# Kernel tuning notes

Hardware: AMD Instinct MI355X
Metric: run time of the kernel (lower is better)

The kernel has to match this reference:

```python
import jax, jax.numpy as jnp
import numpy as np

B, H, SQ, SKV, D = 2, 16, 2048, 2048, 64
SCALE = 8  # sqrt(head_dim)


def setup_inputs() -> dict:
    key = jax.random.key(0)
    kq, kk, kv, km = jax.random.split(key, 4)
    q = jax.random.normal(kq, (B, H, SQ, D), dtype=jnp.float32)
    k = jax.random.normal(kk, (B, H, SKV, D), dtype=jnp.float32)
    v = jax.random.normal(kv, (B, H, SKV, D), dtype=jnp.float32)
    mask = jax.random.normal(km, (1, 1, SQ, SKV), dtype=jnp.float32)
    return {"q": q, "k": k, "v": v, "mask": mask, "scale": SCALE}


def reference(q, k, v, mask, scale):
    # scores: [B, H, SQ, SKV]
    scores = jnp.einsum("bhqd,bhkd->bhqk", q, k) / scale
    scores = scores + mask  # broadcast additive mask
    probs = jax.nn.softmax(scores, axis=-1)
    # hidden: [B, H, SQ, D]
    return jnp.einsum("bhqk,bhkd->bhqd", probs, v)
```

## Files before the change

kernel.cpp:

```cpp
#include <hip/hip_runtime.h>
#include <hip/hip_bf16.h>

#define NB 2
#define NH 16
#define NSQ 2048
#define NSKV 2048
#define ND 64
#define NT (NSKV / 64)
#define LOG2E 1.4426950408889634f
#define BHSTRIDE (NSKV * ND)

typedef __attribute__((ext_vector_type(8))) short bf16x8;
typedef __attribute__((ext_vector_type(4))) float f32x4;
typedef __attribute__((address_space(1))) const unsigned gas_u32;
typedef __attribute__((address_space(3))) unsigned las_u32;

__device__ __forceinline__ short f2bf(float x) {
  union { float f; unsigned u; } c; c.f = x;
  unsigned r = c.u + 0x7fffu + ((c.u >> 16) & 1u);
  return (short)(r >> 16);
}
__device__ __forceinline__ unsigned pack_bf2(float lo, float hi) {
  union { __hip_bfloat162 h; unsigned u; } c;
  c.h = __float22bfloat162_rn(float2{lo, hi});
  return c.u;
}
__device__ __forceinline__ float u2f(unsigned u) {
  union { unsigned u; float f; } c; c.u = u; return c.f;
}
__device__ __forceinline__ float exp2_fast(float x) {
#if __has_builtin(__builtin_amdgcn_exp2f)
  return __builtin_amdgcn_exp2f(x);
#else
  return exp2f(x);
#endif
}

__device__ __forceinline__ int kvmap(int x) {
  return (x & 3) | (((x >> 4) & 1) << 2) | (((x >> 2) & 1) << 3)
       | (((x >> 3) & 1) << 4) | (x & 32);
}

__global__ void prep_all(const float* __restrict__ K, const float* __restrict__ V,
                         const float* __restrict__ M, short* __restrict__ Kp,
                         short* __restrict__ Vp, unsigned short* __restrict__ Mt) {
  __shared__ float T[64][65];
  const int tile = blockIdx.x;
  const int bh   = blockIdx.y;
  const int kv0  = tile * 64;
  const int t    = (int)threadIdx.x;

  {
    const float* src = V + ((size_t)bh * NSKV + kv0) * ND;
#pragma unroll
    for (int i = 0; i < 4; ++i) {
      float4 v = *(const float4*)(src + (size_t)((t >> 4) + 16 * i) * ND + (t & 15) * 4);
      T[(t >> 4) + 16 * i][(t & 15) * 4 + 0] = v.x;
      T[(t >> 4) + 16 * i][(t & 15) * 4 + 1] = v.y;
      T[(t >> 4) + 16 * i][(t & 15) * 4 + 2] = v.z;
      T[(t >> 4) + 16 * i][(t & 15) * 4 + 3] = v.w;
    }
    __syncthreads();
    const int d = t >> 2, c = t & 3;
    bf16x8 w0, w1;
#pragma unroll
    for (int j = 0; j < 8; ++j) w0[j] = f2bf(T[c * 16 + j][d]);
#pragma unroll
    for (int j = 0; j < 8; ++j) w1[j] = f2bf(T[c * 16 + 8 + j][d]);
    const int frag  = (d >> 4) * 2 + (c >> 1);
    const int lane0 = (((2 * c) & 3) << 4) | (d & 15);
    const int lane1 = (((2 * c + 1) & 3) << 4) | (d & 15);
    short* dstb = Vp + (size_t)bh * BHSTRIDE + (size_t)tile * 4096 + frag * 512;
    *(bf16x8*)(dstb + lane0 * 8) = w0;
    *(bf16x8*)(dstb + lane1 * 8) = w1;
  }

#pragma unroll
  for (int h = 0; h < 2; ++h) {
    const int u    = t + h * 256;
    const int nt   = u >> 7, kc = (u >> 6) & 1, lane = u & 63;
    const int prow = nt * 16 + (lane & 15);
    const float* src = K + ((size_t)bh * NSKV + kv0 + kvmap(prow)) * ND
                         + kc * 32 + (lane >> 4) * 8;
    float4 a = *(const float4*)src, b = *(const float4*)(src + 4);
    bf16x8 w;
    w[0]=f2bf(a.x); w[1]=f2bf(a.y); w[2]=f2bf(a.z); w[3]=f2bf(a.w);
    w[4]=f2bf(b.x); w[5]=f2bf(b.y); w[6]=f2bf(b.z); w[7]=f2bf(b.w);
    *(bf16x8*)(Kp + (size_t)bh * BHSTRIDE + (size_t)tile * 4096 + u * 8) = w;
  }

  {
    const int rl = t >> 4, c = t & 15;
    const int nt   = 2 * (c >> 3) + (c & 1);
    const int lq   = (c >> 1) & 3;
    const int lane = lq * 16 + rl;
#pragma unroll
    for (int i = 0; i < 4; ++i) {
      const int qt  = bh * 4 + i;
      const int row = qt * 16 + rl;
      float4 v = *(const float4*)(M + (size_t)row * NSKV + tile * 64 + c * 4);
      ushort4 o;
      o.x = (unsigned short)f2bf(LOG2E * v.x);
      o.y = (unsigned short)f2bf(LOG2E * v.y);
      o.z = (unsigned short)f2bf(LOG2E * v.z);
      o.w = (unsigned short)f2bf(LOG2E * v.w);
      *(ushort4*)(Mt + (((size_t)qt * 32 + tile) * 64 + lane) * 16 + nt * 4) = o;
    }
  }
}

__global__ __launch_bounds__(256, 2)
void attn_fwd(const float* __restrict__ Q, const short* __restrict__ Kp,
              const short* __restrict__ Vp, const unsigned short* __restrict__ Mt,
              const void* __restrict__ scale_p, float* __restrict__ O)
{
  const int lin = (int)blockIdx.x + ((int)blockIdx.y << 4);
  const int swz = ((lin & 7) << 6) | (lin >> 3);
  const int qb  = swz & 15;
  const int bh  = swz >> 4;

  const int tid = (int)threadIdx.x;
  const int wv  = tid >> 6;
  const int ln  = tid & 63;
  const int l16 = ln & 15;
  const int lq  = ln >> 4;

  float scale_v;
  {
    union { int i; float f; } u;
    u.i = ((const int*)scale_p)[0];
    float af = fabsf(u.f);
    scale_v = (af >= 1e-6f && af <= 1e6f) ? u.f : (float)u.i;
  }
  const float qmul = LOG2E / scale_v;

  const int q0 = qb * 128;
  const short* Kb = Kp + (size_t)bh * BHSTRIDE;
  const short* Vb = Vp + (size_t)bh * BHSTRIDE;

  __shared__ short Kl[2][4096];
  __shared__ short Vl[2][4096];

  bf16x8 qf[2][2];
#pragma unroll
  for (int qs = 0; qs < 2; ++qs) {
    const float* qrow = Q + ((size_t)bh * NSQ + q0 + wv * 32 + qs * 16 + l16) * ND;
#pragma unroll
    for (int kc = 0; kc < 2; ++kc) {
      const float4* p = (const float4*)(qrow + kc * 32 + lq * 8);
      float4 a = p[0], b = p[1];
      bf16x8 f;
      f[0]=f2bf(a.x*qmul); f[1]=f2bf(a.y*qmul); f[2]=f2bf(a.z*qmul); f[3]=f2bf(a.w*qmul);
      f[4]=f2bf(b.x*qmul); f[5]=f2bf(b.y*qmul); f[6]=f2bf(b.z*qmul); f[7]=f2bf(b.w*qmul);
      qf[qs][kc] = f;
    }
  }

  f32x4 oa[2][4];
  f32x4 lacc[2];
#pragma unroll
  for (int qs = 0; qs < 2; ++qs) {
#pragma unroll
    for (int dt = 0; dt < 4; ++dt) { f32x4 z = {0.f,0.f,0.f,0.f}; oa[qs][dt] = z; }
    f32x4 z = {0.f,0.f,0.f,0.f}; lacc[qs] = z;
  }

  bf16x8 ones;
#pragma unroll
  for (int j = 0; j < 8; ++j) ones[j] = (short)0x3F80;

  const unsigned short* M0 = Mt + (size_t)(qb * 8 + wv * 2) * 32768 + (size_t)ln * 16;
  const unsigned short* M1 = M0 + 32768;

  auto mload = [&](int t, float4* mf0, float4* mf1) {
    const unsigned short* p0 = M0 + (size_t)t * 1024;
    const unsigned short* p1 = M1 + (size_t)t * 1024;
    uint4 a0 = *(const uint4*)p0, b0 = *(const uint4*)(p0 + 8);
    uint4 a1 = *(const uint4*)p1, b1 = *(const uint4*)(p1 + 8);
    const unsigned u0[8] = {a0.x,a0.y,a0.z,a0.w,b0.x,b0.y,b0.z,b0.w};
    const unsigned u1[8] = {a1.x,a1.y,a1.z,a1.w,b1.x,b1.y,b1.z,b1.w};
#pragma unroll
    for (int nt = 0; nt < 4; ++nt) {
      mf0[nt] = float4{u2f(u0[nt*2] << 16), u2f(u0[nt*2] & 0xffff0000u),
                       u2f(u0[nt*2+1] << 16), u2f(u0[nt*2+1] & 0xffff0000u)};
      mf1[nt] = float4{u2f(u1[nt*2] << 16), u2f(u1[nt*2] & 0xffff0000u),
                       u2f(u1[nt*2+1] << 16), u2f(u1[nt*2+1] & 0xffff0000u)};
    }
  };

  auto stage = [&](int t, int buf) {
    const short* ks = Kb + (size_t)t * 4096;
    const short* vs = Vb + (size_t)t * 4096;
#pragma unroll
    for (int i = 0; i < 2; ++i) {
      const int chunk = wv * 2 + i;
      __builtin_amdgcn_global_load_lds((gas_u32*)(ks + chunk * 512 + ln * 8),
                                       (las_u32*)&Kl[buf][chunk * 512], 16, 0, 0);
      __builtin_amdgcn_global_load_lds((gas_u32*)(vs + chunk * 512 + ln * 8),
                                       (las_u32*)&Vl[buf][chunk * 512], 16, 0, 0);
    }
  };

  auto subtile = [&](bf16x8 (&kf)[4][2], bf16x8 (&vf)[4][2], int qs, float4* mf) {
    f32x4 s[4];
    __builtin_amdgcn_s_setprio(1);
#pragma unroll
    for (int nt = 0; nt < 4; ++nt) {
      f32x4 a = *(const f32x4*)&mf[nt];
      a = __builtin_amdgcn_mfma_f32_16x16x32_bf16(kf[nt][0], qf[qs][0], a, 0, 0, 0);
      a = __builtin_amdgcn_mfma_f32_16x16x32_bf16(kf[nt][1], qf[qs][1], a, 0, 0, 0);
      s[nt] = a;
    }
    __builtin_amdgcn_s_setprio(0);
#pragma unroll
    for (int nt = 0; nt < 4; ++nt) {
      s[nt][0] = exp2_fast(s[nt][0]);
      s[nt][1] = exp2_fast(s[nt][1]);
      s[nt][2] = exp2_fast(s[nt][2]);
      s[nt][3] = exp2_fast(s[nt][3]);
    }
    bf16x8 pa[2];
#pragma unroll
    for (int kc = 0; kc < 2; ++kc) {
      union { unsigned u[4]; bf16x8 v; } w;
      w.u[0] = pack_bf2(s[2*kc][0],   s[2*kc][1]);
      w.u[1] = pack_bf2(s[2*kc][2],   s[2*kc][3]);
      w.u[2] = pack_bf2(s[2*kc+1][0], s[2*kc+1][1]);
      w.u[3] = pack_bf2(s[2*kc+1][2], s[2*kc+1][3]);
      pa[kc] = w.v;
    }
    __builtin_amdgcn_s_setprio(1);
#pragma unroll
    for (int kc = 0; kc < 2; ++kc) {
#pragma unroll
      for (int dt = 0; dt < 4; ++dt)
        oa[qs][dt] = __builtin_amdgcn_mfma_f32_16x16x32_bf16(pa[kc], vf[dt][kc], oa[qs][dt], 0, 0, 0);
      lacc[qs] = __builtin_amdgcn_mfma_f32_16x16x32_bf16(pa[kc], ones, lacc[qs], 0, 0, 0);
    }
    __builtin_amdgcn_s_setprio(0);
  };

  auto tile = [&](int t, int buf, float4 (&mc0)[4], float4 (&mc1)[4],
                  float4 (&mn0)[4], float4 (&mn1)[4]) {
    if (t + 1 < NT) {
      stage(t + 1, buf ^ 1);
      mload(t + 1, mn0, mn1);
    }
    bf16x8 kf[4][2], vf[4][2];
#pragma unroll
    for (int nt = 0; nt < 4; ++nt)
#pragma unroll
      for (int kc = 0; kc < 2; ++kc) {
        kf[nt][kc] = *(const bf16x8*)&Kl[buf][(nt * 2 + kc) * 512 + ln * 8];
        vf[nt][kc] = *(const bf16x8*)&Vl[buf][(nt * 2 + kc) * 512 + ln * 8];
      }
    subtile(kf, vf, 0, mc0);
    subtile(kf, vf, 1, mc1);
    __syncthreads();
  };

  float4 mA0[4], mA1[4], mB0[4], mB1[4];
  stage(0, 0);
  mload(0, mA0, mA1);
  __syncthreads();

  for (int t = 0; t < NT; t += 2) {
    tile(t,     0, mA0, mA1, mB0, mB1);
    tile(t + 1, 1, mB0, mB1, mA0, mA1);
  }

#pragma unroll
  for (int qs = 0; qs < 2; ++qs)
#pragma unroll
    for (int r = 0; r < 4; ++r) {
      const float inv = 1.0f / lacc[qs][r];
      float* orow = O + ((size_t)bh * NSQ + q0 + wv * 32 + qs * 16 + lq * 4 + r) * ND;
#pragma unroll
      for (int dt = 0; dt < 4; ++dt)
        orow[dt * 16 + l16] = oa[qs][dt][r] * inv;
    }
}

extern "C" void kernel_launch(void* const* d_in, const int* in_sizes, int n_in,
                              void* d_out, int out_size, void* d_ws, size_t ws_size,
                              hipStream_t stream) {
  const float* q     = (const float*)d_in[0];
  const float* k     = (const float*)d_in[1];
  const float* v     = (const float*)d_in[2];
  const float* mask  = (const float*)d_in[3];
  const void*  scale = (const void*)d_in[4];
  float* out = (float*)d_out;

  const size_t NELEM = (size_t)NB * NH * NSKV * ND;
  short* Kpk = (short*)d_ws;
  short* Vpk = Kpk + NELEM;
  unsigned short* Mtl = (unsigned short*)(Vpk + NELEM);

  prep_all<<<dim3(NSKV / 64, NB * NH), 256, 0, stream>>>(k, v, mask, Kpk, Vpk, Mtl);

  dim3 grid(NSQ / 128, NB * NH);
  attn_fwd<<<grid, 256, 0, stream>>>(q, Kpk, Vpk, Mtl, scale, out);
}
```

Baseline: 67.44 us.

## Switch attention to single-wave blocks loading K/V directly into registers

Replaces the 256-thread, LDS-staged attention kernel with 64-thread blocks. Each wave handles 64 query rows and loads K/V fragments straight from global memory into registers, double-buffered across tiles, so there is no shared memory and no block barriers. The block-to-(bh, q) mapping is swizzled so blocks sharing a head land close together, relying on L2 to supply the K/V reuse that LDS sharing used to provide. Per-wave K/V traffic rises and register pressure grows with four query subtiles, and setprio hints are dropped.

```diff
diff --git a/kernel.cpp b/kernel.cpp
--- a/kernel.cpp
+++ b/kernel.cpp
@@ -12,8 +12,6 @@
 
 typedef __attribute__((ext_vector_type(8))) short bf16x8;
 typedef __attribute__((ext_vector_type(4))) float f32x4;
-typedef __attribute__((address_space(1))) const unsigned gas_u32;
-typedef __attribute__((address_space(3))) unsigned las_u32;
 
 __device__ __forceinline__ short f2bf(float x) {
   union { float f; unsigned u; } c; c.f = x;
@@ -109,19 +107,17 @@
   }
 }
 
-__global__ __launch_bounds__(256, 2)
+__global__ __launch_bounds__(64, 1)
 void attn_fwd(const float* __restrict__ Q, const short* __restrict__ Kp,
               const short* __restrict__ Vp, const unsigned short* __restrict__ Mt,
               const void* __restrict__ scale_p, float* __restrict__ O)
 {
-  const int lin = (int)blockIdx.x + ((int)blockIdx.y << 4);
-  const int swz = ((lin & 7) << 6) | (lin >> 3);
-  const int qb  = swz & 15;
-  const int bh  = swz >> 4;
-
-  const int tid = (int)threadIdx.x;
-  const int wv  = tid >> 6;
-  const int ln  = tid & 63;
+  const int lin = (int)blockIdx.x;
+  const int idx = lin >> 3;
+  const int bh  = (lin & 7) * 4 + (idx >> 5);
+  const int qb  = idx & 31;
+
+  const int ln  = (int)threadIdx.x & 63;
   const int l16 = ln & 15;
   const int lq  = ln >> 4;
 
@@ -134,17 +130,14 @@
   }
   const float qmul = LOG2E / scale_v;
 
-  const int q0 = qb * 128;
+  const int q0 = qb * 64;
   const short* Kb = Kp + (size_t)bh * BHSTRIDE;
   const short* Vb = Vp + (size_t)bh * BHSTRIDE;
 
-  __shared__ short Kl[2][4096];
-  __shared__ short Vl[2][4096];
-
-  bf16x8 qf[2][2];
-#pragma unroll
-  for (int qs = 0; qs < 2; ++qs) {
-    const float* qrow = Q + ((size_t)bh * NSQ + q0 + wv * 32 + qs * 16 + l16) * ND;
+  bf16x8 qf[4][2];
+#pragma unroll
+  for (int qs = 0; qs < 4; ++qs) {
+    const float* qrow = Q + ((size_t)bh * NSQ + q0 + qs * 16 + l16) * ND;
 #pragma unroll
     for (int kc = 0; kc < 2; ++kc) {
       const float4* p = (const float4*)(qrow + kc * 32 + lq * 8);
@@ -156,10 +149,10 @@
     }
   }
 
-  f32x4 oa[2][4];
-  f32x4 lacc[2];
-#pragma unroll
-  for (int qs = 0; qs < 2; ++qs) {
+  f32x4 oa[4][4];
+  f32x4 lacc[4];
+#pragma unroll
+  for (int qs = 0; qs < 4; ++qs) {
 #pragma unroll
     for (int dt = 0; dt < 4; ++dt) { f32x4 z = {0.f,0.f,0.f,0.f}; oa[qs][dt] = z; }
     f32x4 z = {0.f,0.f,0.f,0.f}; lacc[qs] = z;
@@ -169,49 +162,43 @@
 #pragma unroll
   for (int j = 0; j < 8; ++j) ones[j] = (short)0x3F80;
 
-  const unsigned short* M0 = Mt + (size_t)(qb * 8 + wv * 2) * 32768 + (size_t)ln * 16;
-  const unsigned short* M1 = M0 + 32768;
-
-  auto mload = [&](int t, float4* mf0, float4* mf1) {
-    const unsigned short* p0 = M0 + (size_t)t * 1024;
-    const unsigned short* p1 = M1 + (size_t)t * 1024;
-    uint4 a0 = *(const uint4*)p0, b0 = *(const uint4*)(p0 + 8);
-    uint4 a1 = *(const uint4*)p1, b1 = *(const uint4*)(p1 + 8);
-    const unsigned u0[8] = {a0.x,a0.y,a0.z,a0.w,b0.x,b0.y,b0.z,b0.w};
-    const unsigned u1[8] = {a1.x,a1.y,a1.z,a1.w,b1.x,b1.y,b1.z,b1.w};
+  const unsigned short* Mq = Mt + (size_t)(qb * 4) * 32768 + (size_t)ln * 16;
+
+  union MU { uint4 q[2]; unsigned u[8]; };
+
+  auto mload = [&](int t, MU (&m)[4]) {
+#pragma unroll
+    for (int qs = 0; qs < 4; ++qs) {
+      const unsigned short* p = Mq + (size_t)qs * 32768 + (size_t)t * 1024;
+      m[qs].q[0] = *(const uint4*)p;
+      m[qs].q[1] = *(const uint4*)(p + 8);
+    }
+  };
+
+  auto kvload = [&](int t, bf16x8 (&kf)[4][2], bf16x8 (&vf)[4][2]) {
+    const short* kt = Kb + (size_t)t * 4096 + ln * 8;
+    const short* vt = Vb + (size_t)t * 4096 + ln * 8;
+#pragma unroll
+    for (int f = 0; f < 8; ++f) {
+      kf[f >> 1][f & 1] = *(const bf16x8*)(kt + f * 512);
+      vf[f >> 1][f & 1] = *(const bf16x8*)(vt + f * 512);
+    }
+  };
+
+  auto qk = [&](bf16x8 (&kf)[4][2], int qs, const MU& m, f32x4 (&s)[4]) {
 #pragma unroll
     for (int nt = 0; nt < 4; ++nt) {
-      mf0[nt] = float4{u2f(u0[nt*2] << 16), u2f(u0[nt*2] & 0xffff0000u),
-                       u2f(u0[nt*2+1] << 16), u2f(u0[nt*2+1] & 0xffff0000u)};
-      mf1[nt] = float4{u2f(u1[nt*2] << 16), u2f(u1[nt*2] & 0xffff0000u),
-                       u2f(u1[nt*2+1] << 16), u2f(u1[nt*2+1] & 0xffff0000u)};
-    }
-  };
-
-  auto stage = [&](int t, int buf) {
-    const short* ks = Kb + (size_t)t * 4096;
-    const short* vs = Vb + (size_t)t * 4096;
-#pragma unroll
-    for (int i = 0; i < 2; ++i) {
-      const int chunk = wv * 2 + i;
-      __builtin_amdgcn_global_load_lds((gas_u32*)(ks + chunk * 512 + ln * 8),
-                                       (las_u32*)&Kl[buf][chunk * 512], 16, 0, 0);
-      __builtin_amdgcn_global_load_lds((gas_u32*)(vs + chunk * 512 + ln * 8),
-                                       (las_u32*)&Vl[buf][chunk * 512], 16, 0, 0);
-    }
-  };
-
-  auto subtile = [&](bf16x8 (&kf)[4][2], bf16x8 (&vf)[4][2], int qs, float4* mf) {
-    f32x4 s[4];
-    __builtin_amdgcn_s_setprio(1);
-#pragma unroll
-    for (int nt = 0; nt < 4; ++nt) {
-      f32x4 a = *(const f32x4*)&mf[nt];
+      const unsigned w0 = m.u[nt * 2], w1 = m.u[nt * 2 + 1];
+      f32x4 a;
+      a[0] = u2f(w0 << 16); a[1] = u2f(w0 & 0xffff0000u);
+      a[2] = u2f(w1 << 16); a[3] = u2f(w1 & 0xffff0000u);
       a = __builtin_amdgcn_mfma_f32_16x16x32_bf16(kf[nt][0], qf[qs][0], a, 0, 0, 0);
       a = __builtin_amdgcn_mfma_f32_16x16x32_bf16(kf[nt][1], qf[qs][1], a, 0, 0, 0);
       s[nt] = a;
     }
-    __builtin_amdgcn_s_setprio(0);
+  };
+
+  auto smpack = [&](f32x4 (&s)[4], bf16x8 (&pa)[2]) {
 #pragma unroll
     for (int nt = 0; nt < 4; ++nt) {
       s[nt][0] = exp2_fast(s[nt][0]);
@@ -219,7 +206,6 @@
       s[nt][2] = exp2_fast(s[nt][2]);
       s[nt][3] = exp2_fast(s[nt][3]);
     }
-    bf16x8 pa[2];
 #pragma unroll
     for (int kc = 0; kc < 2; ++kc) {
       union { unsigned u[4]; bf16x8 v; } w;
@@ -229,7 +215,9 @@
       w.u[3] = pack_bf2(s[2*kc+1][2], s[2*kc+1][3]);
       pa[kc] = w.v;
     }
-    __builtin_amdgcn_s_setprio(1);
+  };
+
+  auto pv = [&](bf16x8 (&vf)[4][2], int qs, bf16x8 (&pa)[2]) {
 #pragma unroll
     for (int kc = 0; kc < 2; ++kc) {
 #pragma unroll
@@ -237,44 +225,46 @@
         oa[qs][dt] = __builtin_amdgcn_mfma_f32_16x16x32_bf16(pa[kc], vf[dt][kc], oa[qs][dt], 0, 0, 0);
       lacc[qs] = __builtin_amdgcn_mfma_f32_16x16x32_bf16(pa[kc], ones, lacc[qs], 0, 0, 0);
     }
-    __builtin_amdgcn_s_setprio(0);
-  };
-
-  auto tile = [&](int t, int buf, float4 (&mc0)[4], float4 (&mc1)[4],
-                  float4 (&mn0)[4], float4 (&mn1)[4]) {
+  };
+
+  auto tile = [&](int t, bf16x8 (&kfc)[4][2], bf16x8 (&vfc)[4][2], MU (&mcc)[4],
+                  bf16x8 (&kfn)[4][2], bf16x8 (&vfn)[4][2], MU (&mcn)[4]) {
     if (t + 1 < NT) {
-      stage(t + 1, buf ^ 1);
-      mload(t + 1, mn0, mn1);
-    }
-    bf16x8 kf[4][2], vf[4][2];
-#pragma unroll
-    for (int nt = 0; nt < 4; ++nt)
-#pragma unroll
-      for (int kc = 0; kc < 2; ++kc) {
-        kf[nt][kc] = *(const bf16x8*)&Kl[buf][(nt * 2 + kc) * 512 + ln * 8];
-        vf[nt][kc] = *(const bf16x8*)&Vl[buf][(nt * 2 + kc) * 512 + ln * 8];
-      }
-    subtile(kf, vf, 0, mc0);
-    subtile(kf, vf, 1, mc1);
-    __syncthreads();
-  };
-
-  float4 mA0[4], mA1[4], mB0[4], mB1[4];
-  stage(0, 0);
-  mload(0, mA0, mA1);
-  __syncthreads();
+      kvload(t + 1, kfn, vfn);
+      mload(t + 1, mcn);
+    }
+    f32x4 s0[4], s1[4];
+    bf16x8 pa0[2], pa1[2];
+    qk(kfc, 0, mcc[0], s0);
+    qk(kfc, 1, mcc[1], s1);
+    smpack(s0, pa0);
+    pv(vfc, 0, pa0);
+    smpack(s1, pa1);
+    pv(vfc, 1, pa1);
+    qk(kfc, 2, mcc[2], s0);
+    qk(kfc, 3, mcc[3], s1);
+    smpack(s0, pa0);
+    pv(vfc, 2, pa0);
+    smpack(s1, pa1);
+    pv(vfc, 3, pa1);
+  };
+
+  bf16x8 kA[4][2], vA[4][2], kB[4][2], vB[4][2];
+  MU mA[4], mB[4];
+  kvload(0, kA, vA);
+  mload(0, mA);
 
   for (int t = 0; t < NT; t += 2) {
-    tile(t,     0, mA0, mA1, mB0, mB1);
-    tile(t + 1, 1, mB0, mB1, mA0, mA1);
-  }
-
-#pragma unroll
-  for (int qs = 0; qs < 2; ++qs)
+    tile(t,     kA, vA, mA, kB, vB, mB);
+    tile(t + 1, kB, vB, mB, kA, vA, mA);
+  }
+
+#pragma unroll
+  for (int qs = 0; qs < 4; ++qs)
 #pragma unroll
     for (int r = 0; r < 4; ++r) {
       const float inv = 1.0f / lacc[qs][r];
-      float* orow = O + ((size_t)bh * NSQ + q0 + wv * 32 + qs * 16 + lq * 4 + r) * ND;
+      float* orow = O + ((size_t)bh * NSQ + q0 + qs * 16 + lq * 4 + r) * ND;
 #pragma unroll
       for (int dt = 0; dt < 4; ++dt)
         orow[dt * 16 + l16] = oa[qs][dt][r] * inv;
@@ -298,6 +288,5 @@
 
   prep_all<<<dim3(NSKV / 64, NB * NH), 256, 0, stream>>>(k, v, mask, Kpk, Vpk, Mtl);
 
-  dim3 grid(NSQ / 128, NB * NH);
-  attn_fwd<<<grid, 256, 0, stream>>>(q, Kpk, Vpk, Mtl, scale, out);
-}
+  attn_fwd<<<dim3(1024), 64, 0, stream>>>(q, Kpk, Vpk, Mtl, scale, out);
+}
```

Measured after the change: 88.94 us. 1.32x slower.

## Split KV tile across wave pairs with split-K reduction through LDS

Applied to the files above, without the earlier changes.

Waves are regrouped into two pairs, each pair covering 64 query rows. Within a pair, each wave handles half of every 64-key tile, so each wave reads half the K/V fragments from LDS but computes four query subtiles. Partial output and row-sum accumulators are combined at the end through LDS scratch with extra barriers. This cuts per-wave LDS fragment traffic and mask loads per tile, at the cost of twice the accumulator registers and a final reduction step.

```diff
diff --git a/kernel.cpp b/kernel.cpp
--- a/kernel.cpp
+++ b/kernel.cpp
@@ -121,6 +121,8 @@
 
   const int tid = (int)threadIdx.x;
   const int wv  = tid >> 6;
+  const int g   = wv >> 1;
+  const int h   = wv & 1;
   const int ln  = tid & 63;
   const int l16 = ln & 15;
   const int lq  = ln >> 4;
@@ -138,13 +140,13 @@
   const short* Kb = Kp + (size_t)bh * BHSTRIDE;
   const short* Vb = Vp + (size_t)bh * BHSTRIDE;
 
-  __shared__ short Kl[2][4096];
-  __shared__ short Vl[2][4096];
-
-  bf16x8 qf[2][2];
-#pragma unroll
-  for (int qs = 0; qs < 2; ++qs) {
-    const float* qrow = Q + ((size_t)bh * NSQ + q0 + wv * 32 + qs * 16 + l16) * ND;
+  __shared__ __align__(16) short Kl[2][4096];
+  __shared__ __align__(16) short Vl[2][4096];
+
+  bf16x8 qf[4][2];
+#pragma unroll
+  for (int qs = 0; qs < 4; ++qs) {
+    const float* qrow = Q + ((size_t)bh * NSQ + q0 + g * 64 + qs * 16 + l16) * ND;
 #pragma unroll
     for (int kc = 0; kc < 2; ++kc) {
       const float4* p = (const float4*)(qrow + kc * 32 + lq * 8);
@@ -156,10 +158,10 @@
     }
   }
 
-  f32x4 oa[2][4];
-  f32x4 lacc[2];
-#pragma unroll
-  for (int qs = 0; qs < 2; ++qs) {
+  f32x4 oa[4][4];
+  f32x4 lacc[4];
+#pragma unroll
+  for (int qs = 0; qs < 4; ++qs) {
 #pragma unroll
     for (int dt = 0; dt < 4; ++dt) { f32x4 z = {0.f,0.f,0.f,0.f}; oa[qs][dt] = z; }
     f32x4 z = {0.f,0.f,0.f,0.f}; lacc[qs] = z;
@@ -169,23 +171,13 @@
 #pragma unroll
   for (int j = 0; j < 8; ++j) ones[j] = (short)0x3F80;
 
-  const unsigned short* M0 = Mt + (size_t)(qb * 8 + wv * 2) * 32768 + (size_t)ln * 16;
-  const unsigned short* M1 = M0 + 32768;
-
-  auto mload = [&](int t, float4* mf0, float4* mf1) {
-    const unsigned short* p0 = M0 + (size_t)t * 1024;
-    const unsigned short* p1 = M1 + (size_t)t * 1024;
-    uint4 a0 = *(const uint4*)p0, b0 = *(const uint4*)(p0 + 8);
-    uint4 a1 = *(const uint4*)p1, b1 = *(const uint4*)(p1 + 8);
-    const unsigned u0[8] = {a0.x,a0.y,a0.z,a0.w,b0.x,b0.y,b0.z,b0.w};
-    const unsigned u1[8] = {a1.x,a1.y,a1.z,a1.w,b1.x,b1.y,b1.z,b1.w};
-#pragma unroll
-    for (int nt = 0; nt < 4; ++nt) {
-      mf0[nt] = float4{u2f(u0[nt*2] << 16), u2f(u0[nt*2] & 0xffff0000u),
-                       u2f(u0[nt*2+1] << 16), u2f(u0[nt*2+1] & 0xffff0000u)};
-      mf1[nt] = float4{u2f(u1[nt*2] << 16), u2f(u1[nt*2] & 0xffff0000u),
-                       u2f(u1[nt*2+1] << 16), u2f(u1[nt*2+1] & 0xffff0000u)};
-    }
+  const unsigned short* Mq = Mt + (size_t)(qb * 8 + g * 4) * 32768
+                                + (size_t)ln * 16 + h * 8;
+
+  auto mload = [&](int t, uint4 (&m)[4]) {
+#pragma unroll
+    for (int qs = 0; qs < 4; ++qs)
+      m[qs] = *(const uint4*)(Mq + (size_t)qs * 32768 + (size_t)t * 1024);
   };
 
   auto stage = [&](int t, int buf) {
@@ -201,84 +193,113 @@
     }
   };
 
-  auto subtile = [&](bf16x8 (&kf)[4][2], bf16x8 (&vf)[4][2], int qs, float4* mf) {
-    f32x4 s[4];
-    __builtin_amdgcn_s_setprio(1);
-#pragma unroll
-    for (int nt = 0; nt < 4; ++nt) {
-      f32x4 a = *(const f32x4*)&mf[nt];
-      a = __builtin_amdgcn_mfma_f32_16x16x32_bf16(kf[nt][0], qf[qs][0], a, 0, 0, 0);
-      a = __builtin_amdgcn_mfma_f32_16x16x32_bf16(kf[nt][1], qf[qs][1], a, 0, 0, 0);
-      s[nt] = a;
-    }
-    __builtin_amdgcn_s_setprio(0);
-#pragma unroll
-    for (int nt = 0; nt < 4; ++nt) {
-      s[nt][0] = exp2_fast(s[nt][0]);
-      s[nt][1] = exp2_fast(s[nt][1]);
-      s[nt][2] = exp2_fast(s[nt][2]);
-      s[nt][3] = exp2_fast(s[nt][3]);
-    }
-    bf16x8 pa[2];
-#pragma unroll
-    for (int kc = 0; kc < 2; ++kc) {
-      union { unsigned u[4]; bf16x8 v; } w;
-      w.u[0] = pack_bf2(s[2*kc][0],   s[2*kc][1]);
-      w.u[1] = pack_bf2(s[2*kc][2],   s[2*kc][3]);
-      w.u[2] = pack_bf2(s[2*kc+1][0], s[2*kc+1][1]);
-      w.u[3] = pack_bf2(s[2*kc+1][2], s[2*kc+1][3]);
-      pa[kc] = w.v;
-    }
-    __builtin_amdgcn_s_setprio(1);
-#pragma unroll
-    for (int kc = 0; kc < 2; ++kc) {
-#pragma unroll
-      for (int dt = 0; dt < 4; ++dt)
-        oa[qs][dt] = __builtin_amdgcn_mfma_f32_16x16x32_bf16(pa[kc], vf[dt][kc], oa[qs][dt], 0, 0, 0);
-      lacc[qs] = __builtin_amdgcn_mfma_f32_16x16x32_bf16(pa[kc], ones, lacc[qs], 0, 0, 0);
-    }
-    __builtin_amdgcn_s_setprio(0);
-  };
-
-  auto tile = [&](int t, int buf, float4 (&mc0)[4], float4 (&mc1)[4],
-                  float4 (&mn0)[4], float4 (&mn1)[4]) {
+  auto tile = [&](int t, int buf, uint4 (&mc)[4], uint4 (&mn)[4]) {
     if (t + 1 < NT) {
       stage(t + 1, buf ^ 1);
-      mload(t + 1, mn0, mn1);
-    }
-    bf16x8 kf[4][2], vf[4][2];
-#pragma unroll
-    for (int nt = 0; nt < 4; ++nt)
-#pragma unroll
-      for (int kc = 0; kc < 2; ++kc) {
-        kf[nt][kc] = *(const bf16x8*)&Kl[buf][(nt * 2 + kc) * 512 + ln * 8];
-        vf[nt][kc] = *(const bf16x8*)&Vl[buf][(nt * 2 + kc) * 512 + ln * 8];
-      }
-    subtile(kf, vf, 0, mc0);
-    subtile(kf, vf, 1, mc1);
+      mload(t + 1, mn);
+    }
+    bf16x8 kf[2][2], vf[4];
+#pragma unroll
+    for (int l = 0; l < 2; ++l)
+#pragma unroll
+      for (int kc = 0; kc < 2; ++kc)
+        kf[l][kc] = *(const bf16x8*)&Kl[buf][((2 * h + l) * 2 + kc) * 512 + ln * 8];
+#pragma unroll
+    for (int dt = 0; dt < 4; ++dt)
+      vf[dt] = *(const bf16x8*)&Vl[buf][(dt * 2 + h) * 512 + ln * 8];
+
+#pragma unroll
+    for (int qs = 0; qs < 4; ++qs) {
+      const uint4 m = mc[qs];
+      f32x4 s0, s1;
+      s0[0] = u2f(m.x << 16); s0[1] = u2f(m.x & 0xffff0000u);
+      s0[2] = u2f(m.y << 16); s0[3] = u2f(m.y & 0xffff0000u);
+      s1[0] = u2f(m.z << 16); s1[1] = u2f(m.z & 0xffff0000u);
+      s1[2] = u2f(m.w << 16); s1[3] = u2f(m.w & 0xffff0000u);
+      __builtin_amdgcn_s_setprio(1);
+      s0 = __builtin_amdgcn_mfma_f32_16x16x32_bf16(kf[0][0], qf[qs][0], s0, 0, 0, 0);
+      s0 = __builtin_amdgcn_mfma_f32_16x16x32_bf16(kf[0][1], qf[qs][1], s0, 0, 0, 0);
+      s1 = __builtin_amdgcn_mfma_f32_16x16x32_bf16(kf[1][0], qf[qs][0], s1, 0, 0, 0);
+      s1 = __builtin_amdgcn_mfma_f32_16x16x32_bf16(kf[1][1], qf[qs][1], s1, 0, 0, 0);
+      __builtin_amdgcn_s_setprio(0);
+
+      s0[0] = exp2_fast(s0[0]); s0[1] = exp2_fast(s0[1]);
+      s0[2] = exp2_fast(s0[2]); s0[3] = exp2_fast(s0[3]);
+      s1[0] = exp2_fast(s1[0]); s1[1] = exp2_fast(s1[1]);
+      s1[2] = exp2_fast(s1[2]); s1[3] = exp2_fast(s1[3]);
+
+      union { unsigned u[4]; bf16x8 v; } w;
+      w.u[0] = pack_bf2(s0[0], s0[1]);
+      w.u[1] = pack_bf2(s0[2], s0[3]);
+      w.u[2] = pack_bf2(s1[0], s1[1]);
+      w.u[3] = pack_bf2(s1[2], s1[3]);
+      const bf16x8 pa = w.v;
+
+      __builtin_amdgcn_s_setprio(1);
+#pragma unroll
+      for (int dt = 0; dt < 4; ++dt)
+        oa[qs][dt] = __builtin_amdgcn_mfma_f32_16x16x32_bf16(pa, vf[dt], oa[qs][dt], 0, 0, 0);
+      lacc[qs] = __builtin_amdgcn_mfma_f32_16x16x32_bf16(pa, ones, lacc[qs], 0, 0, 0);
+      __builtin_amdgcn_s_setprio(0);
+    }
+
     __syncthreads();
   };
 
-  float4 mA0[4], mA1[4], mB0[4], mB1[4];
+  uint4 mA[4], mB[4];
   stage(0, 0);
-  mload(0, mA0, mA1);
+  mload(0, mA);
   __syncthreads();
 
   for (int t = 0; t < NT; t += 2) {
-    tile(t,     0, mA0, mA1, mB0, mB1);
-    tile(t + 1, 1, mB0, mB1, mA0, mA1);
-  }
-
-#pragma unroll
-  for (int qs = 0; qs < 2; ++qs)
-#pragma unroll
-    for (int r = 0; r < 4; ++r) {
-      const float inv = 1.0f / lacc[qs][r];
-      float* orow = O + ((size_t)bh * NSQ + q0 + wv * 32 + qs * 16 + lq * 4 + r) * ND;
+    tile(t,     0, mA, mB);
+    tile(t + 1, 1, mB, mA);
+  }
+
+  float* scr = g ? (float*)&Vl[0][0] : (float*)&Kl[0][0];
+  if (h == 1) {
+#pragma unroll
+    for (int qs = 0; qs < 4; ++qs)
 #pragma unroll
       for (int dt = 0; dt < 4; ++dt)
-        orow[dt * 16 + l16] = oa[qs][dt][r] * inv;
-    }
+        *((f32x4*)scr + ((qs * 4 + dt) * 64 + ln)) = oa[qs][dt];
+  }
+  __syncthreads();
+  if (h == 0) {
+#pragma unroll
+    for (int qs = 0; qs < 4; ++qs)
+#pragma unroll
+      for (int dt = 0; dt < 4; ++dt) {
+        f32x4 p = *((const f32x4*)scr + ((qs * 4 + dt) * 64 + ln));
+        oa[qs][dt][0] += p[0]; oa[qs][dt][1] += p[1];
+        oa[qs][dt][2] += p[2]; oa[qs][dt][3] += p[3];
+      }
+  }
+  __syncthreads();
+  if (h == 1) {
+#pragma unroll
+    for (int qs = 0; qs < 4; ++qs)
+      *((f32x4*)scr + (qs * 64 + ln)) = lacc[qs];
+  }
+  __syncthreads();
+  if (h == 0) {
+#pragma unroll
+    for (int qs = 0; qs < 4; ++qs) {
+      f32x4 p = *((const f32x4*)scr + (qs * 64 + ln));
+      lacc[qs][0] += p[0]; lacc[qs][1] += p[1];
+      lacc[qs][2] += p[2]; lacc[qs][3] += p[3];
+    }
+#pragma unroll
+    for (int qs = 0; qs < 4; ++qs)
+#pragma unroll
+      for (int r = 0; r < 4; ++r) {
+        const float inv = 1.0f / lacc[qs][r];
+        float* orow = O + ((size_t)bh * NSQ + q0 + g * 64 + qs * 16 + lq * 4 + r) * ND;
+#pragma unroll
+        for (int dt = 0; dt < 4; ++dt)
+          orow[dt * 16 + l16] = oa[qs][dt][r] * inv;
+      }
+  }
 }
 
 extern "C" void kernel_launch(void* const* d_in, const int* in_sizes, int n_in,
```

Result: slower. 69.08 us (+2.4%).
